# Performance work log

Measured on AMD Instinct MI355X. Metric: run time of the kernel, lower is better.

The kernel has to match this reference:

```python
import jax, jax.numpy as jnp
import numpy as np

EPS = 1e-8
LRELU_SLOPE = 0.2
ACT_GAIN = float(np.sqrt(2.0))  # def_gain for lrelu
GAIN = 1.0                      # forward default
CLAMP = 256.0


def setup_inputs() -> dict:
    key = jax.random.key(0)
    k1, k2 = jax.random.split(key)
    x = jax.random.normal(k1, (8, 128, 32, 32, 32), dtype=jnp.float32)
    weight = jax.random.normal(k2, (128, 128, 3, 3, 3), dtype=jnp.float32)
    bias = jnp.zeros((128,), dtype=jnp.float32)
    return {"x": x, "weight": weight, "bias": bias}


def _modulated_conv3d(x, weight, styles, padding, demodulate=True):
    # x: [B, Cin, D, H, W], weight: [Cout, Cin, kd, kh, kw], styles: [B, Cin]
    w = weight[None] * styles[:, None, :, None, None, None]  # [B, Cout, Cin, kd, kh, kw]
    if demodulate:
        dcoefs = jax.lax.rsqrt(jnp.sum(jnp.square(w), axis=(2, 3, 4, 5)) + EPS)  # [B, Cout]
        w = w * dcoefs[:, :, None, None, None, None]
    pad = [(padding, padding)] * 3

    def per_sample(xi, wi):
        # xi: [Cin, D, H, W], wi: [Cout, Cin, kd, kh, kw]
        return jax.lax.conv_general_dilated(
            xi[None], wi, window_strides=(1, 1, 1), padding=pad,
            dimension_numbers=("NCDHW", "OIDHW", "NCDHW"))[0]

    return jax.vmap(per_sample)(x, w)  # [B, Cout, D, H, W]


def reference(x, weight, bias):
    padding = weight.shape[-1] // 2
    styles = jnp.ones((x.shape[0], weight.shape[1]), dtype=x.dtype)
    y = _modulated_conv3d(x, weight, styles, padding)
    y = jax.nn.leaky_relu(y + bias[None, :, None, None, None], LRELU_SLOPE)
    # clamp_gain(act, act_gain*gain, 256*gain)
    return jnp.clip(y * (ACT_GAIN * GAIN), -CLAMP * GAIN, CLAMP * GAIN)
```

## Files before the change

### kernel.cpp

```cpp
#include <hip/hip_runtime.h>

typedef short bf16x8 __attribute__((ext_vector_type(8)));
typedef float f32x4  __attribute__((ext_vector_type(4)));
typedef unsigned short u16;

static __device__ __forceinline__ u16 f2bf(float f) {
    unsigned int u = __builtin_bit_cast(unsigned int, f);
    u += 0x7FFFu + ((u >> 16) & 1u);
    return (u16)(u >> 16);
}

static __device__ __forceinline__ void gload_lds16(const void* g, void* l) {
    __builtin_amdgcn_global_load_lds((const __attribute__((address_space(1))) void*)g,
                                     (__attribute__((address_space(3))) void*)l, 16, 0, 0);
}

__global__ __launch_bounds__(256) void prep_w_k(const float* __restrict__ w,
                                                u16* __restrict__ wn) {
    const int co = blockIdx.x;
    const int t  = threadIdx.x;
    const float* wc = w + co * 3456;
    float s = 0.f;
    for (int i = t; i < 3456; i += 256) { float v = wc[i]; s += v * v; }
#pragma unroll
    for (int off = 32; off; off >>= 1) s += __shfl_down(s, off);
    __shared__ float red[4];
    __shared__ float dsh;
    if ((t & 63) == 0) red[t >> 6] = s;
    __syncthreads();
    if (t == 0) dsh = rsqrtf(red[0] + red[1] + red[2] + red[3] + 1e-8f);
    __syncthreads();
    const float d = dsh;
    for (int i = t; i < 3456; i += 256) {
        int ci = i / 27, tap = i - ci * 27;
        float v = wc[i] * d;
        wn[((tap * 4 + (ci >> 5)) * 128 + co) * 32 + (ci & 31)] = f2bf(v);
    }
}

__global__ __launch_bounds__(256) void xpose_k(const float* __restrict__ x,
                                               u16* __restrict__ xt) {
    const int bid = blockIdx.x;
    const int b = bid >> 10, d = (bid >> 5) & 31, h = bid & 31;
    const int t = threadIdx.x;
    const int w = t & 31, cg = t >> 5;
    const int base_dhw = d * 1024 + h * 32 + w;
#pragma unroll
    for (int r = 0; r < 2; ++r) {
        int g = cg + r * 8;
        const float* src = x + ((size_t)(b * 128 + g * 8) << 15) + base_dhw;
        bf16x8 pk;
#pragma unroll
        for (int j = 0; j < 8; ++j) pk[j] = (short)f2bf(src[(size_t)j << 15]);
        *(bf16x8*)&xt[((size_t)((b * 16 + g) << 15) + base_dhw) * 8] = pk;
    }
}

#define KSX 1048576
#define KSW 4096
#define RB  12288
__global__ __launch_bounds__(512, 2) void conv_mx(
    const u16* __restrict__ wsb, const float* __restrict__ bias,
    float* __restrict__ out) {
    __shared__ __align__(16) u16 lds[3 * RB];
    const u16* xt = wsb + 524288;
    const u16* wn = wsb + 512;
    const u16* zp = wsb;

    const int t = threadIdx.x, lane = t & 63, wid = t >> 6;
    const int ll = lane & 15, g = lane >> 4;
    const int mslice = wid >> 1, ncol = wid & 1;

    int wg = ((blockIdx.x & 7) << 7) | (blockIdx.x >> 3);
    const int b = wg >> 7, dt = (wg >> 3) & 15, ht = wg & 7;
    const int d0 = dt * 2, h0 = ht * 4;

    const int pos0 = mslice * 64 + ll;
    const int xro = pos0 * 32 + ((g ^ ((pos0 >> 1) & 3)) * 8);
    const int co0 = ncol * 64 + ll;
    const int wro = 8192 + co0 * 32 + ((g ^ ((co0 >> 1) & 3)) * 8);

    const int posA = wid * 32 + (lane >> 2);
    const int slot = lane & 3;
    const int pdA = posA >> 7, phA = (posA >> 5) & 3, wA = posA & 31;
    const int gA = slot ^ ((posA >> 1) & 3);
    const int wco = wid * 16 + (lane >> 2);
    const u16* wsrc = wn + wco * 32 + ((slot ^ ((wco >> 1) & 3)) * 8);

    f32x4 acc[4][4];
#pragma unroll
    for (int i = 0; i < 4; ++i)
#pragma unroll
        for (int j = 0; j < 4; ++j) acc[i][j] = (f32x4){0.f, 0.f, 0.f, 0.f};

    int od_s = 0, oh_s = 0, ow_s = 0, cc_s = 0;
    const u16* xsA = xt; bool okA = false, okB = false;

    bf16x8 xa[4], wa[4], xb[4], wb[4];

#define DO_STAGE(SB) { \
    if (cc_s == 0) { \
        int Dx = d0 + pdA - 1 + od_s, Hx = h0 + phA - 1 + oh_s, Wx = wA - 1 + ow_s; \
        bool dh_ = ((unsigned)Dx < 32u) && ((unsigned)Hx < 32u); \
        okA = dh_ && ((unsigned)Wx < 32u); \
        okB = dh_ && (Wx < 16); \
        xsA = xt + (long)((b * 16 + gA) * 32768 + Dx * 1024 + Hx * 32 + Wx) * 8; } \
    gload_lds16(okA ? (const void*)xsA : (const void*)zp, (void*)&lds[(SB)*RB + wid*1024]); \
    gload_lds16(okB ? (const void*)(xsA + 128) : (const void*)zp, (void*)&lds[(SB)*RB + wid*1024 + 512]); \
    gload_lds16((const void*)wsrc, (void*)&lds[(SB)*RB + 8192 + wid*512]); \
    xsA += KSX; wsrc += KSW; \
    if (++cc_s == 4) { cc_s = 0; \
        if (++ow_s == 3) { ow_s = 0; if (++oh_s == 3) { oh_s = 0; ++od_s; } } } }

#define RDFRAG(RD, XF, WF) { \
    _Pragma("unroll") for (int mf = 0; mf < 4; ++mf) \
        XF[mf] = *(const bf16x8*)&lds[(RD)*RB + xro + mf * 512]; \
    _Pragma("unroll") for (int nf = 0; nf < 4; ++nf) \
        WF[nf] = *(const bf16x8*)&lds[(RD)*RB + wro + nf * 512]; }

#define MFMACL(XF, WF) { \
    __builtin_amdgcn_s_setprio(1); \
    _Pragma("unroll") for (int mf = 0; mf < 4; ++mf) \
    _Pragma("unroll") for (int nf = 0; nf < 4; ++nf) \
        acc[mf][nf] = __builtin_amdgcn_mfma_f32_16x16x32_bf16(WF[nf], XF[mf], acc[mf][nf], 0, 0, 0); \
    __builtin_amdgcn_s_setprio(0); }

#define KSTEP(RD, SB, CX, CW, NX, NW, DOST, VMSTR) { \
    RDFRAG(RD, NX, NW); \
    if (DOST) DO_STAGE(SB); \
    MFMACL(CX, CW); \
    asm volatile("s_waitcnt lgkmcnt(0)" ::: "memory"); \
    asm volatile("s_waitcnt " VMSTR ::: "memory"); \
    asm volatile("s_barrier" ::: "memory"); }

    DO_STAGE(0); DO_STAGE(1); DO_STAGE(2);
    asm volatile("s_waitcnt vmcnt(6)" ::: "memory");
    asm volatile("s_barrier" ::: "memory");
    RDFRAG(0, xa, wa);
    asm volatile("s_waitcnt lgkmcnt(0)" ::: "memory");
    asm volatile("s_waitcnt vmcnt(3)" ::: "memory");
    asm volatile("s_barrier" ::: "memory");

    for (int m = 0; m < 17; ++m) {
        KSTEP(1, 0, xa, wa, xb, wb, 1, "vmcnt(3)");
        KSTEP(2, 1, xb, wb, xa, wa, 1, "vmcnt(3)");
        KSTEP(0, 2, xa, wa, xb, wb, 1, "vmcnt(3)");
        KSTEP(1, 0, xb, wb, xa, wa, 1, "vmcnt(3)");
        KSTEP(2, 1, xa, wa, xb, wb, 1, "vmcnt(3)");
        KSTEP(0, 2, xb, wb, xa, wa, 1, "vmcnt(3)");
    }
    KSTEP(1, 0, xa, wa, xb, wb, 1, "vmcnt(3)");
    KSTEP(2, 1, xb, wb, xa, wa, 1, "vmcnt(3)");
    KSTEP(0, 2, xa, wa, xb, wb, 1, "vmcnt(3)");
    KSTEP(1, 0, xb, wb, xa, wa, 0, "vmcnt(0)");
    KSTEP(2, 0, xa, wa, xb, wb, 0, "vmcnt(0)");
    MFMACL(xb, wb);

    const int pd = mslice >> 1, phb = (mslice & 1) * 2;
#pragma unroll
    for (int nf = 0; nf < 4; ++nf) {
        f32x4 bb = *(const f32x4*)&bias[ncol * 64 + nf * 16 + g * 4];
#pragma unroll
        for (int mf = 0; mf < 4; ++mf) {
            const int wq = (mf & 1) * 16 + ll;
            const int hh = h0 + phb + (mf >> 1);
            float* orow = out + ((size_t)(b * 128 + ncol * 64 + nf * 16 + g * 4) << 15)
                          + (d0 + pd) * 1024 + hh * 32 + wq;
#pragma unroll
            for (int q = 0; q < 4; ++q) {
                float v = acc[mf][nf][q] + bb[q];
                v = v > 0.f ? v : v * 0.2f;
                v *= 1.41421356237f;
                v = fminf(fmaxf(v, -256.f), 256.f);
                orow[(size_t)q << 15] = v;
            }
        }
    }
#undef DO_STAGE
#undef RDFRAG
#undef MFMACL
#undef KSTEP
}

#define NPOS 544
__global__ __launch_bounds__(256, 4) void conv_fb(
    const float* __restrict__ x, const u16* __restrict__ wn,
    const float* __restrict__ bias, float* __restrict__ out) {
    __shared__ __align__(16) u16 lds[NPOS * 32];
    float* ldsf = reinterpret_cast<float*>(lds);
    const int t = threadIdx.x;
    const int lane = t & 63;
    const int wid  = t >> 6;
    const int wr   = wid >> 1;
    const int wcn  = wid & 1;
    const int ll   = lane & 15;
    const int g    = lane >> 4;
    const int bid = blockIdx.x;
    const int b  = bid >> 8;
    const int dt = (bid >> 4) & 15, ht = bid & 15;
    const int d0 = dt * 2, h0 = ht * 2;
    const int sw  = t & 31;
    const int sg  = (t >> 5) & 3;
    const int rhi = t >> 7;
    f32x4 acc[4][4];
#pragma unroll
    for (int i = 0; i < 4; ++i)
#pragma unroll
        for (int j = 0; j < 4; ++j) acc[i][j] = (f32x4){0.f, 0.f, 0.f, 0.f};
    float bv[4][4];
#pragma unroll
    for (int nf = 0; nf < 4; ++nf) {
        f32x4 bb = *(const f32x4*)&bias[wcn * 64 + nf * 16 + g * 4];
#pragma unroll
        for (int q = 0; q < 4; ++q) bv[nf][q] = bb[q];
    }
    if (t < 128) {
        int pi  = t >> 2;
        int row = pi >> 1;
        int pos = row * 34 + (pi & 1) * 33;
        bf16x8 z = {0, 0, 0, 0, 0, 0, 0, 0};
        *(bf16x8*)&lds[pos * 32 + (t & 3) * 8] = z;
    }
    for (int c = 0; c < 4; ++c) {
        if (c) __syncthreads();
#pragma unroll
        for (int p = 0; p < 8; ++p) {
            int rowid = p * 2 + rhi;
            int pd = rowid >> 2, ph = rowid & 3;
            int d = d0 - 1 + pd, h = h0 - 1 + ph;
            bool ok = ((unsigned)d < 32u) && ((unsigned)h < 32u);
            const float* src = x + (((b * 128 + c * 32 + sg * 8) * 32 + d) * 32 + h) * 32 + sw;
            float v[8];
#pragma unroll
            for (int j = 0; j < 8; ++j) v[j] = ok ? src[j * 32768] : 0.f;
            bf16x8 pk;
#pragma unroll
            for (int j = 0; j < 8; ++j) pk[j] = (short)f2bf(v[j]);
            int pos = rowid * 34 + sw + 1;
            int sl = sg ^ ((pos >> 1) & 3);
            *(bf16x8*)&lds[pos * 32 + sl * 8] = pk;
        }
        __syncthreads();
        const u16* wbase = wn + c * 4096 + ((wcn * 64 + ll) * 32 + g * 8);
        bf16x8 wf[4];
#pragma unroll
        for (int nf = 0; nf < 4; ++nf) wf[nf] = *(const bf16x8*)&wbase[nf * 512];
#pragma unroll
        for (int tap = 0; tap < 27; ++tap) {
            const int od = tap / 9, oh = (tap / 3) % 3, ow = tap % 3;
            bf16x8 wfn[4];
            if (tap < 26) {
#pragma unroll
                for (int nf = 0; nf < 4; ++nf)
                    wfn[nf] = *(const bf16x8*)&wbase[(tap + 1) * 16384 + nf * 512];
            }
            bf16x8 xf[4];
#pragma unroll
            for (int mf = 0; mf < 4; ++mf) {
                int pos = ((wr + od) * 4 + (mf >> 1) + oh) * 34 + (mf & 1) * 16 + ll + ow;
                int sl = g ^ ((pos >> 1) & 3);
                xf[mf] = *(const bf16x8*)&lds[pos * 32 + sl * 8];
            }
            __builtin_amdgcn_s_setprio(1);
#pragma unroll
            for (int mf = 0; mf < 4; ++mf)
#pragma unroll
                for (int nf = 0; nf < 4; ++nf)
                    acc[mf][nf] = __builtin_amdgcn_mfma_f32_16x16x32_bf16(
                        wf[nf], xf[mf], acc[mf][nf], 0, 0, 0);
            __builtin_amdgcn_s_setprio(0);
            if (tap < 26) {
#pragma unroll
                for (int nf = 0; nf < 4; ++nf) wf[nf] = wfn[nf];
            }
        }
    }
#pragma unroll
    for (int p = 0; p < 4; ++p) {
        const int dd = p >> 1, hh = p & 1;
        __syncthreads();
        if (wr == dd) {
#pragma unroll
            for (int whalf = 0; whalf < 2; ++whalf) {
                const int mf = hh * 2 + whalf;
#pragma unroll
                for (int nf = 0; nf < 4; ++nf) {
#pragma unroll
                    for (int q = 0; q < 4; ++q) {
                        const int co = wcn * 64 + nf * 16 + g * 4 + q;
                        float v = acc[mf][nf][q] + bv[nf][q];
                        v = v > 0.f ? v : v * 0.2f;
                        v *= 1.41421356237f;
                        v = fminf(fmaxf(v, -256.f), 256.f);
                        ldsf[co * 33 + whalf * 16 + ll] = v;
                    }
                }
            }
        }
        __syncthreads();
#pragma unroll
        for (int it = 0; it < 4; ++it) {
            const int row = it * 32 + (t >> 3);
            const int ls  = t & 7;
            f32x4 v = *(f32x4*)&ldsf[row * 33 + ls * 4];
            *(f32x4*)&out[(size_t)(b * 128 + row) * 32768 +
                          (d0 + dd) * 1024 + (h0 + hh) * 32 + ls * 4] = v;
        }
    }
}

extern "C" void kernel_launch(void* const* d_in, const int* in_sizes, int n_in,
                              void* d_out, int out_size, void* d_ws, size_t ws_size,
                              hipStream_t stream) {
    const float* x    = (const float*)d_in[0];
    const float* w    = (const float*)d_in[1];
    const float* bias = (const float*)d_in[2];
    float* out        = (float*)d_out;
    u16* wsb          = (u16*)d_ws;

    hipMemsetAsync(d_ws, 0, 1024, stream);
    prep_w_k<<<128, 256, 0, stream>>>(w, wsb + 512);

    if (ws_size >= 68157440ull) {
        xpose_k<<<8192, 256, 0, stream>>>(x, wsb + 524288);
        conv_mx<<<1024, 512, 0, stream>>>(wsb, bias, out);
    } else {
        conv_fb<<<2048, 256, 0, stream>>>(x, wsb + 512, bias, out);
    }
}
```

Before: 291.7 us.

## Load weight fragments directly from global into registers instead of via LDS

Weight fragments for the MFMA loop are now read straight from global memory (L2/L1 cached) into registers one k-step ahead, rather than staged through LDS with global_load_lds and read back. This shrinks the LDS ring buffer per stage and removes LDS write/read traffic for weights. The vmcnt waits are retuned to match the new count of outstanding loads. The risk is that global weight reads are more redundant across waves and have longer latency, which may be exposed, and the waits now also stall on the register loads.

```diff
diff --git a/kernel.cpp b/kernel.cpp
--- a/kernel.cpp
+++ b/kernel.cpp
@@ -58,7 +58,7 @@
 
 #define KSX 1048576
 #define KSW 4096
-#define RB  12288
+#define RB  8192
 __global__ __launch_bounds__(512, 2) void conv_mx(
     const u16* __restrict__ wsb, const float* __restrict__ bias,
     float* __restrict__ out) {
@@ -77,15 +77,13 @@
 
     const int pos0 = mslice * 64 + ll;
     const int xro = pos0 * 32 + ((g ^ ((pos0 >> 1) & 3)) * 8);
-    const int co0 = ncol * 64 + ll;
-    const int wro = 8192 + co0 * 32 + ((g ^ ((co0 >> 1) & 3)) * 8);
+
+    const u16* wptr = wn + (ncol * 64 + ll) * 32 + g * 8;
 
     const int posA = wid * 32 + (lane >> 2);
     const int slot = lane & 3;
     const int pdA = posA >> 7, phA = (posA >> 5) & 3, wA = posA & 31;
     const int gA = slot ^ ((posA >> 1) & 3);
-    const int wco = wid * 16 + (lane >> 2);
-    const u16* wsrc = wn + wco * 32 + ((slot ^ ((wco >> 1) & 3)) * 8);
 
     f32x4 acc[4][4];
 #pragma unroll
@@ -97,6 +95,11 @@
     const u16* xsA = xt; bool okA = false, okB = false;
 
     bf16x8 xa[4], wa[4], xb[4], wb[4];
+
+#define WLOAD(WF) { \
+    _Pragma("unroll") for (int nf = 0; nf < 4; ++nf) \
+        WF[nf] = *(const bf16x8*)&wptr[nf * 512]; \
+    wptr += KSW; }
 
 #define DO_STAGE(SB) { \
     if (cc_s == 0) { \
@@ -107,16 +110,13 @@
         xsA = xt + (long)((b * 16 + gA) * 32768 + Dx * 1024 + Hx * 32 + Wx) * 8; } \
     gload_lds16(okA ? (const void*)xsA : (const void*)zp, (void*)&lds[(SB)*RB + wid*1024]); \
     gload_lds16(okB ? (const void*)(xsA + 128) : (const void*)zp, (void*)&lds[(SB)*RB + wid*1024 + 512]); \
-    gload_lds16((const void*)wsrc, (void*)&lds[(SB)*RB + 8192 + wid*512]); \
-    xsA += KSX; wsrc += KSW; \
+    xsA += KSX; \
     if (++cc_s == 4) { cc_s = 0; \
         if (++ow_s == 3) { ow_s = 0; if (++oh_s == 3) { oh_s = 0; ++od_s; } } } }
 
-#define RDFRAG(RD, XF, WF) { \
+#define RDFRAG(RD, XF) { \
     _Pragma("unroll") for (int mf = 0; mf < 4; ++mf) \
-        XF[mf] = *(const bf16x8*)&lds[(RD)*RB + xro + mf * 512]; \
-    _Pragma("unroll") for (int nf = 0; nf < 4; ++nf) \
-        WF[nf] = *(const bf16x8*)&lds[(RD)*RB + wro + nf * 512]; }
+        XF[mf] = *(const bf16x8*)&lds[(RD)*RB + xro + mf * 512]; }
 
 #define MFMACL(XF, WF) { \
     __builtin_amdgcn_s_setprio(1); \
@@ -125,8 +125,9 @@
         acc[mf][nf] = __builtin_amdgcn_mfma_f32_16x16x32_bf16(WF[nf], XF[mf], acc[mf][nf], 0, 0, 0); \
     __builtin_amdgcn_s_setprio(0); }
 
-#define KSTEP(RD, SB, CX, CW, NX, NW, DOST, VMSTR) { \
-    RDFRAG(RD, NX, NW); \
+#define KSTEP(RD, SB, CX, CW, NX, NW, DOST, DOW, VMSTR) { \
+    if (DOW) WLOAD(NW); \
+    RDFRAG(RD, NX); \
     if (DOST) DO_STAGE(SB); \
     MFMACL(CX, CW); \
     asm volatile("s_waitcnt lgkmcnt(0)" ::: "memory"); \
@@ -134,26 +135,26 @@
     asm volatile("s_barrier" ::: "memory"); }
 
     DO_STAGE(0); DO_STAGE(1); DO_STAGE(2);
-    asm volatile("s_waitcnt vmcnt(6)" ::: "memory");
+    WLOAD(wa);
+    asm volatile("s_waitcnt vmcnt(0)" ::: "memory");
     asm volatile("s_barrier" ::: "memory");
-    RDFRAG(0, xa, wa);
+    RDFRAG(0, xa);
     asm volatile("s_waitcnt lgkmcnt(0)" ::: "memory");
-    asm volatile("s_waitcnt vmcnt(3)" ::: "memory");
     asm volatile("s_barrier" ::: "memory");
 
     for (int m = 0; m < 17; ++m) {
-        KSTEP(1, 0, xa, wa, xb, wb, 1, "vmcnt(3)");
-        KSTEP(2, 1, xb, wb, xa, wa, 1, "vmcnt(3)");
-        KSTEP(0, 2, xa, wa, xb, wb, 1, "vmcnt(3)");
-        KSTEP(1, 0, xb, wb, xa, wa, 1, "vmcnt(3)");
-        KSTEP(2, 1, xa, wa, xb, wb, 1, "vmcnt(3)");
-        KSTEP(0, 2, xb, wb, xa, wa, 1, "vmcnt(3)");
-    }
-    KSTEP(1, 0, xa, wa, xb, wb, 1, "vmcnt(3)");
-    KSTEP(2, 1, xb, wb, xa, wa, 1, "vmcnt(3)");
-    KSTEP(0, 2, xa, wa, xb, wb, 1, "vmcnt(3)");
-    KSTEP(1, 0, xb, wb, xa, wa, 0, "vmcnt(0)");
-    KSTEP(2, 0, xa, wa, xb, wb, 0, "vmcnt(0)");
+        KSTEP(1, 0, xa, wa, xb, wb, 1, 1, "vmcnt(2)");
+        KSTEP(2, 1, xb, wb, xa, wa, 1, 1, "vmcnt(2)");
+        KSTEP(0, 2, xa, wa, xb, wb, 1, 1, "vmcnt(2)");
+        KSTEP(1, 0, xb, wb, xa, wa, 1, 1, "vmcnt(2)");
+        KSTEP(2, 1, xa, wa, xb, wb, 1, 1, "vmcnt(2)");
+        KSTEP(0, 2, xb, wb, xa, wa, 1, 1, "vmcnt(2)");
+    }
+    KSTEP(1, 0, xa, wa, xb, wb, 1, 1, "vmcnt(2)");
+    KSTEP(2, 1, xb, wb, xa, wa, 1, 1, "vmcnt(2)");
+    KSTEP(0, 2, xa, wa, xb, wb, 1, 1, "vmcnt(2)");
+    KSTEP(1, 0, xb, wb, xa, wa, 0, 1, "vmcnt(0)");
+    KSTEP(2, 0, xa, wa, xb, wb, 0, 1, "vmcnt(0)");
     MFMACL(xb, wb);
 
     const int pd = mslice >> 1, phb = (mslice & 1) * 2;
@@ -176,6 +177,7 @@
             }
         }
     }
+#undef WLOAD
 #undef DO_STAGE
 #undef RDFRAG
 #undef MFMACL
```

After: 518.2 us. 1.78x slower.

## Load activation fragments directly from global into registers, bypassing LDS staging

Applied to the files above, without the earlier changes.

Activation tiles are no longer staged through LDS with global_load_lds. Each lane now loads its bf16x8 fragments straight from global memory into registers, with zero-pointer padding for halo and boundary cases. Only weights stay triple-buffered in LDS, which shrinks shared memory per block. The aim is to cut LDS traffic and footprint, at the cost of more global load latency exposed in the register path and some redundant loads across waves.

```diff
diff --git a/kernel.cpp b/kernel.cpp
--- a/kernel.cpp
+++ b/kernel.cpp
@@ -58,11 +58,11 @@
 
 #define KSX 1048576
 #define KSW 4096
-#define RB  12288
+#define WRB 4096
 __global__ __launch_bounds__(512, 2) void conv_mx(
     const u16* __restrict__ wsb, const float* __restrict__ bias,
     float* __restrict__ out) {
-    __shared__ __align__(16) u16 lds[3 * RB];
+    __shared__ __align__(16) u16 lds[3 * WRB];
     const u16* xt = wsb + 524288;
     const u16* wn = wsb + 512;
     const u16* zp = wsb;
@@ -75,48 +75,58 @@
     const int b = wg >> 7, dt = (wg >> 3) & 15, ht = wg & 7;
     const int d0 = dt * 2, h0 = ht * 4;
 
-    const int pos0 = mslice * 64 + ll;
-    const int xro = pos0 * 32 + ((g ^ ((pos0 >> 1) & 3)) * 8);
     const int co0 = ncol * 64 + ll;
-    const int wro = 8192 + co0 * 32 + ((g ^ ((co0 >> 1) & 3)) * 8);
-
-    const int posA = wid * 32 + (lane >> 2);
+    const int wro = co0 * 32 + ((g ^ ((co0 >> 1) & 3)) * 8);
+
+    const int wco = wid * 16 + (lane >> 2);
     const int slot = lane & 3;
-    const int pdA = posA >> 7, phA = (posA >> 5) & 3, wA = posA & 31;
-    const int gA = slot ^ ((posA >> 1) & 3);
-    const int wco = wid * 16 + (lane >> 2);
     const u16* wsrc = wn + wco * 32 + ((slot ^ ((wco >> 1) & 3)) * 8);
 
+    const int pd0 = (mslice * 2) >> 2, ph0 = (mslice * 2) & 3;
+
     f32x4 acc[4][4];
 #pragma unroll
     for (int i = 0; i < 4; ++i)
 #pragma unroll
         for (int j = 0; j < 4; ++j) acc[i][j] = (f32x4){0.f, 0.f, 0.f, 0.f};
 
-    int od_s = 0, oh_s = 0, ow_s = 0, cc_s = 0;
-    const u16* xsA = xt; bool okA = false, okB = false;
+    int ccx = 0, owx = 0, ohx = 0, odx = 0;
+    const u16* xb0 = xt; const u16* xb1 = xt;
+    bool rok0 = false, rok1 = false, we0 = false, we1 = false;
 
     bf16x8 xa[4], wa[4], xb[4], wb[4];
 
-#define DO_STAGE(SB) { \
-    if (cc_s == 0) { \
-        int Dx = d0 + pdA - 1 + od_s, Hx = h0 + phA - 1 + oh_s, Wx = wA - 1 + ow_s; \
-        bool dh_ = ((unsigned)Dx < 32u) && ((unsigned)Hx < 32u); \
-        okA = dh_ && ((unsigned)Wx < 32u); \
-        okB = dh_ && (Wx < 16); \
-        xsA = xt + (long)((b * 16 + gA) * 32768 + Dx * 1024 + Hx * 32 + Wx) * 8; } \
-    gload_lds16(okA ? (const void*)xsA : (const void*)zp, (void*)&lds[(SB)*RB + wid*1024]); \
-    gload_lds16(okB ? (const void*)(xsA + 128) : (const void*)zp, (void*)&lds[(SB)*RB + wid*1024 + 512]); \
-    gload_lds16((const void*)wsrc, (void*)&lds[(SB)*RB + 8192 + wid*512]); \
-    xsA += KSX; wsrc += KSW; \
-    if (++cc_s == 4) { cc_s = 0; \
-        if (++ow_s == 3) { ow_s = 0; if (++oh_s == 3) { oh_s = 0; ++od_s; } } } }
-
-#define RDFRAG(RD, XF, WF) { \
-    _Pragma("unroll") for (int mf = 0; mf < 4; ++mf) \
-        XF[mf] = *(const bf16x8*)&lds[(RD)*RB + xro + mf * 512]; \
+#define XLOAD(NX) { \
+    if (ccx == 0) { \
+        int Dx  = d0 + pd0 - 1 + odx; \
+        int Hx0 = h0 + ph0 - 1 + ohx; \
+        bool Dok = ((unsigned)Dx < 32u); \
+        rok0 = Dok && ((unsigned)Hx0 < 32u); \
+        rok1 = Dok && ((unsigned)(Hx0 + 1) < 32u); \
+        xb0 = xt + (long)((b * 16 + g) * 32768 + Dx * 1024 + Hx0 * 32 + (owx - 1)) * 8; \
+        xb1 = xb0 + 256; \
+        we0 = (owx != 0) || (ll != 0); \
+        we1 = (owx != 2) || (ll != 15); \
+    } \
+    const u16* p0 = (rok0 && we0) ? (xb0 + ll * 8)       : zp; \
+    const u16* p1 = (rok0 && we1) ? (xb0 + 128 + ll * 8) : zp; \
+    const u16* p2 = (rok1 && we0) ? (xb1 + ll * 8)       : zp; \
+    const u16* p3 = (rok1 && we1) ? (xb1 + 128 + ll * 8) : zp; \
+    NX[0] = *(const bf16x8*)p0; \
+    NX[1] = *(const bf16x8*)p1; \
+    NX[2] = *(const bf16x8*)p2; \
+    NX[3] = *(const bf16x8*)p3; \
+    xb0 += KSX; xb1 += KSX; \
+    if (++ccx == 4) { ccx = 0; \
+        if (++owx == 3) { owx = 0; if (++ohx == 3) { ohx = 0; ++odx; } } } }
+
+#define WREAD(RD, WF) { \
     _Pragma("unroll") for (int nf = 0; nf < 4; ++nf) \
-        WF[nf] = *(const bf16x8*)&lds[(RD)*RB + wro + nf * 512]; }
+        WF[nf] = *(const bf16x8*)&lds[(RD)*WRB + wro + nf * 512]; }
+
+#define WSTAGE(SB) { \
+    gload_lds16((const void*)wsrc, (void*)&lds[(SB)*WRB + wid * 512]); \
+    wsrc += KSW; }
 
 #define MFMACL(XF, WF) { \
     __builtin_amdgcn_s_setprio(1); \
@@ -126,32 +136,34 @@
     __builtin_amdgcn_s_setprio(0); }
 
 #define KSTEP(RD, SB, CX, CW, NX, NW, DOST, VMSTR) { \
-    RDFRAG(RD, NX, NW); \
-    if (DOST) DO_STAGE(SB); \
+    XLOAD(NX); \
+    WREAD(RD, NW); \
+    __builtin_amdgcn_sched_barrier(0); \
+    if (DOST) WSTAGE(SB); \
     MFMACL(CX, CW); \
     asm volatile("s_waitcnt lgkmcnt(0)" ::: "memory"); \
     asm volatile("s_waitcnt " VMSTR ::: "memory"); \
     asm volatile("s_barrier" ::: "memory"); }
 
-    DO_STAGE(0); DO_STAGE(1); DO_STAGE(2);
-    asm volatile("s_waitcnt vmcnt(6)" ::: "memory");
+    WSTAGE(0); WSTAGE(1); WSTAGE(2);
+    XLOAD(xa);
+    asm volatile("s_waitcnt vmcnt(0)" ::: "memory");
     asm volatile("s_barrier" ::: "memory");
-    RDFRAG(0, xa, wa);
+    WREAD(0, wa);
     asm volatile("s_waitcnt lgkmcnt(0)" ::: "memory");
-    asm volatile("s_waitcnt vmcnt(3)" ::: "memory");
     asm volatile("s_barrier" ::: "memory");
 
     for (int m = 0; m < 17; ++m) {
-        KSTEP(1, 0, xa, wa, xb, wb, 1, "vmcnt(3)");
-        KSTEP(2, 1, xb, wb, xa, wa, 1, "vmcnt(3)");
-        KSTEP(0, 2, xa, wa, xb, wb, 1, "vmcnt(3)");
-        KSTEP(1, 0, xb, wb, xa, wa, 1, "vmcnt(3)");
-        KSTEP(2, 1, xa, wa, xb, wb, 1, "vmcnt(3)");
-        KSTEP(0, 2, xb, wb, xa, wa, 1, "vmcnt(3)");
-    }
-    KSTEP(1, 0, xa, wa, xb, wb, 1, "vmcnt(3)");
-    KSTEP(2, 1, xb, wb, xa, wa, 1, "vmcnt(3)");
-    KSTEP(0, 2, xa, wa, xb, wb, 1, "vmcnt(3)");
+        KSTEP(1, 0, xa, wa, xb, wb, 1, "vmcnt(1)");
+        KSTEP(2, 1, xb, wb, xa, wa, 1, "vmcnt(1)");
+        KSTEP(0, 2, xa, wa, xb, wb, 1, "vmcnt(1)");
+        KSTEP(1, 0, xb, wb, xa, wa, 1, "vmcnt(1)");
+        KSTEP(2, 1, xa, wa, xb, wb, 1, "vmcnt(1)");
+        KSTEP(0, 2, xb, wb, xa, wa, 1, "vmcnt(1)");
+    }
+    KSTEP(1, 0, xa, wa, xb, wb, 1, "vmcnt(1)");
+    KSTEP(2, 1, xb, wb, xa, wa, 1, "vmcnt(1)");
+    KSTEP(0, 2, xa, wa, xb, wb, 1, "vmcnt(1)");
     KSTEP(1, 0, xb, wb, xa, wa, 0, "vmcnt(0)");
     KSTEP(2, 0, xa, wa, xb, wb, 0, "vmcnt(0)");
     MFMACL(xb, wb);
@@ -176,8 +188,9 @@
             }
         }
     }
-#undef DO_STAGE
-#undef RDFRAG
+#undef XLOAD
+#undef WREAD
+#undef WSTAGE
 #undef MFMACL
 #undef KSTEP
 }
```

After: 382.2 us. +31.0%, slower.
